# Kernel optimization log

Measured on AMD Instinct MI355X. Metric: run time of the kernel, lower is better.

The kernel has to match this reference:

```python
import jax, jax.numpy as jnp
import numpy as np

P, L, H = 3, 4, 6          # window size, num scales, num heads
EPS = 1e-5                 # LayerNorm eps (PyTorch default)


def setup_inputs() -> dict:
    key = jax.random.key(0)
    B, T, D = 8, 4096, 768
    ks = jax.random.split(key, 12)
    s = 0.02
    w = lambda k, shape: (jax.random.normal(k, shape, jnp.float32) * s)
    z = lambda n: jnp.zeros((n,), jnp.float32)
    return {
        "x": jax.random.normal(ks[0], (B, T, D), jnp.float32),
        "ln_g": jnp.ones((D,), jnp.float32),
        "ln_b": z(D),
        "qw": w(ks[1], (D, D)), "qb": z(D),
        "kw": w(ks[2], (D, D)), "kb": z(D),
        "vw": w(ks[3], (D, D)), "vb": z(D),
        "inw": w(ks[4], (3 * D, D)), "inb": z(3 * D),   # MHA in_proj
        "mow": w(ks[5], (D, D)), "mob": z(D),            # MHA out_proj
        "ow": w(ks[6], (D, D)), "ob": z(D),              # output_proj
    }


def _layernorm(x, g, b):
    mu = jnp.mean(x, -1, keepdims=True)
    var = jnp.mean((x - mu) ** 2, -1, keepdims=True)
    return (x - mu) * jax.lax.rsqrt(var + EPS) * g + b


def _mha_windows(q, k, v, inw, inb, mow, mob):
    # q,k,v: [B, W, P, D] -- batched tiny attention over all windows at once
    B, W, Pw, D = q.shape
    hd = D // H
    wq, wk, wv = inw[:D], inw[D:2 * D], inw[2 * D:]
    bq, bk, bv = inb[:D], inb[D:2 * D], inb[2 * D:]
    qp = (q @ wq.T + bq).reshape(B, W, Pw, H, hd)
    kp = (k @ wk.T + bk).reshape(B, W, Pw, H, hd)
    vp = (v @ wv.T + bv).reshape(B, W, Pw, H, hd)
    scores = jnp.einsum('bwqhd,bwkhd->bwhqk', qp, kp) / jnp.sqrt(jnp.float32(hd))
    attn = jax.nn.softmax(scores, axis=-1)
    o = jnp.einsum('bwhqk,bwkhd->bwqhd', attn, vp).reshape(B, W, Pw, D)
    return o @ mow.T + mob


def reference(x, ln_g, ln_b, qw, qb, kw, kb, vw, vb, inw, inb, mow, mob, ow, ob):
    B, T, D = x.shape
    xn = _layernorm(x, ln_g, ln_b)
    Q = xn @ qw.T + qb
    K = xn @ kw.T + kb
    V = xn @ vw.T + vb
    acc = jnp.zeros_like(x)
    for kk in range(L):
        scale = P ** kk
        if T < scale:
            continue
        Lp = T // scale
        pool = lambda z: z[:, :Lp * scale].reshape(B, Lp, scale, D).mean(axis=2)
        pQ, pK, pV = pool(Q), pool(K), pool(V)
        W = Lp // P
        if W == 0:
            continue
        win = lambda z: z[:, :W * P].reshape(B, W, P, D)
        o = _mha_windows(win(pQ), win(pK), win(pV), inw, inb, mow, mob)
        so = o.reshape(B, W * P, D)                       # concat of windows
        idx = (jnp.arange(T) * (W * P)) // T              # nearest interp to T
        up = so[:, idx]
        acc = acc + jax.nn.gelu(up, approximate=False)    # exact GELU (torch default)
    out = acc @ ow.T + ob
    return x + out
```

## Files before the change

kernel.cpp:

```cpp
#include <hip/hip_runtime.h>
#include <stdint.h>

typedef short s16x8 __attribute__((ext_vector_type(8)));
typedef float f32x4 __attribute__((ext_vector_type(4)));

__device__ __forceinline__ unsigned short f2bf(float f) {
  unsigned u = __builtin_bit_cast(unsigned, f);
  u = (u + 0x7FFFu + ((u >> 16) & 1u)) >> 16;
  return (unsigned short)u;
}
__device__ __forceinline__ float bf2f(unsigned short h) {
  unsigned u = ((unsigned)h) << 16;
  return __builtin_bit_cast(float, u);
}

__device__ __forceinline__ void gload_lds16(const void* g, void* l) {
  __builtin_amdgcn_global_load_lds((__attribute__((address_space(1))) void*)g,
                                   (__attribute__((address_space(3))) void*)l,
                                   16, 0, 0);
}

__global__ __launch_bounds__(256)
void mstr_prep(const float* __restrict__ qw, const float* __restrict__ kw,
               const float* __restrict__ vw, const float* __restrict__ inw,
               const float* __restrict__ mow, const float* __restrict__ ow,
               const float* __restrict__ inb, const float* __restrict__ qb,
               const float* __restrict__ kb, const float* __restrict__ vb,
               unsigned short* __restrict__ inwB, unsigned short* __restrict__ wT,
               unsigned short* __restrict__ mowB, unsigned short* __restrict__ owB,
               float* __restrict__ bc, float* __restrict__ zb)
{
  const long n1 = 589824;
  __shared__ float tile[32][33];
  int b = blockIdx.x, tid = threadIdx.x;
  if (b < 11520) {
    long i = (long)b * 256 + tid;
    if (i < 3 * n1)      inwB[i] = f2bf(inw[i]);
    else if (i < 4 * n1) mowB[i - 3 * n1] = f2bf(mow[i - 3 * n1]);
    else                 owB[i - 4 * n1] = f2bf(ow[i - 4 * n1]);
  } else if (b < 13248) {
    int z = b - 11520;
    int s = z % 3, r = z / 3;
    int jb = r % 24, kb = r / 24;
    const float* src = (s == 0) ? qw : (s == 1) ? kw : vw;
    unsigned short* dst = wT + (long)s * n1;
    int tx = tid & 31, ty = tid >> 5;
    int j0 = jb * 32, k0 = kb * 32;
#pragma unroll
    for (int i = 0; i < 4; ++i)
      tile[ty + i * 8][tx] = src[(long)(j0 + ty + i * 8) * 768 + k0 + tx];
    __syncthreads();
#pragma unroll
    for (int i = 0; i < 4; ++i)
      dst[(long)(k0 + ty + i * 8) * 768 + j0 + tx] = f2bf(tile[tx][ty + i * 8]);
  } else {
    int gid = (b - 13248) * 256 + tid;
    if (gid < 768) zb[gid] = 0.f;
    int s = gid / 768, c = gid - s * 768;
    const float* bb = (s == 0) ? qb : (s == 1) ? kb : vb;
    const float* wrow = inw + (long)(s * 768 + c) * 768;
    float a = inb[s * 768 + c];
    for (int j = 0; j < 768; ++j) a += bb[j] * wrow[j];
    bc[gid] = a;
  }
}

__global__ __launch_bounds__(256)
void mstr_ln(const float* __restrict__ x, const float* __restrict__ g,
             const float* __restrict__ bt, unsigned short* __restrict__ xn)
{
  int blk = blockIdx.x;
  int bb = blk / 4095, t = blk - bb * 4095;
  const float* xr = x + ((long)bb * 4096 + t) * 768;
  unsigned short* orow = xn + (long)blk * 768;
  int tid = threadIdx.x;
  float v0 = xr[tid], v1 = xr[tid + 256], v2 = xr[tid + 512];
  float s = v0 + v1 + v2;
  float s2 = v0 * v0 + v1 * v1 + v2 * v2;
#pragma unroll
  for (int o = 32; o > 0; o >>= 1) { s += __shfl_down(s, o, 64); s2 += __shfl_down(s2, o, 64); }
  __shared__ float rs[4], rq[4];
  int lane = tid & 63, wid = tid >> 6;
  if (lane == 0) { rs[wid] = s; rq[wid] = s2; }
  __syncthreads();
  float S = rs[0] + rs[1] + rs[2] + rs[3];
  float S2 = rq[0] + rq[1] + rq[2] + rq[3];
  float mu = S * (1.0f / 768.0f);
  float var = S2 * (1.0f / 768.0f) - mu * mu;
  float rstd = rsqrtf(var + 1e-5f);
  __builtin_nontemporal_store(f2bf((v0 - mu) * rstd * g[tid] + bt[tid]), &orow[tid]);
  __builtin_nontemporal_store(f2bf((v1 - mu) * rstd * g[tid + 256] + bt[tid + 256]), &orow[tid + 256]);
  __builtin_nontemporal_store(f2bf((v2 - mu) * rstd * g[tid + 512] + bt[tid + 512]), &orow[tid + 512]);
}

template<int EPI>
__global__ __launch_bounds__(256, 4)
void mstr_gemm(const unsigned short* __restrict__ A, int M,
               const unsigned short* __restrict__ W,
               const float* __restrict__ bias,
               unsigned short* out0, unsigned short* out1, unsigned short* out2,
               float* outf, const float* xadd,
               int rowDiv, int rowStride, int NC, int nwg, long zoff)
{
  __shared__ char smem[49152];
  if (zoff) {
    long zo = (long)blockIdx.y * zoff;
    A += zo; W += zo; out0 += zo; out1 += zo; out2 += zo;
  }
  int orig = blockIdx.x;
  int swq = nwg >> 3, swr = nwg & 7;
  int xcd = orig & 7, sidx = orig >> 3;
  int wg = (xcd < swr ? xcd * (swq + 1) : swr * (swq + 1) + (xcd - swr) * swq) + sidx;
  int rowp = wg / NC, colp = wg - rowp * NC;

  const int tid = threadIdx.x;
  const int lane = tid & 63;
  const int wid = tid >> 6;
  const int wr = wid >> 1, wc = wid & 1;
  const long row0 = (long)rowp * 128;
  const int col0 = colp * 128;

  const int sr = tid >> 2;
  const int sc = (((tid & 3) ^ ((tid >> 3) & 3)) << 3);
  long a0r = row0 + sr;       if (a0r >= M) a0r = M - 1;
  long a1r = row0 + sr + 64;  if (a1r >= M) a1r = M - 1;
  const unsigned short* Ag0 = A + a0r * 768 + sc;
  const unsigned short* Ag1 = A + a1r * 768 + sc;
  const unsigned short* Bg0 = W + (long)(col0 + sr) * 768 + sc;
  const unsigned short* Bg1 = W + (long)(col0 + sr + 64) * 768 + sc;
  char* ldsT = smem + tid * 16;

  const int fr = lane & 15;
  const int g4 = lane >> 4;
  const int cx = ((g4 ^ ((fr >> 1) & 3)) << 4);
  const int aoff = (wr * 64 + fr) * 64 + cx;
  const int boff = 8192 + (wc * 64 + fr) * 64 + cx;

  f32x4 acc[4][4] = {};

#define MSTAGE(T, BO) { \
    gload_lds16(Ag0 + (T) * 32, ldsT + (BO)); \
    gload_lds16(Ag1 + (T) * 32, ldsT + (BO) + 4096); \
    gload_lds16(Bg0 + (T) * 32, ldsT + (BO) + 8192); \
    gload_lds16(Bg1 + (T) * 32, ldsT + (BO) + 12288); }

#define STEP(T) { \
    if ((T) < 23) { \
      MSTAGE((T) + 1, (((T) + 1) % 3) * 16384) \
      asm volatile("s_waitcnt vmcnt(4)" ::: "memory"); \
    } else { \
      asm volatile("s_waitcnt vmcnt(0)" ::: "memory"); \
    } \
    __builtin_amdgcn_s_barrier(); \
    { \
      const char* sb_ = smem + ((T) % 3) * 16384; \
      s16x8 af[4], bfv[4]; \
      _Pragma("unroll") \
      for (int m = 0; m < 4; ++m) af[m] = *(const s16x8*)(sb_ + aoff + m * 1024); \
      _Pragma("unroll") \
      for (int n = 0; n < 4; ++n) bfv[n] = *(const s16x8*)(sb_ + boff + n * 1024); \
      __builtin_amdgcn_s_setprio(1); \
      _Pragma("unroll") \
      for (int m = 0; m < 4; ++m) \
        _Pragma("unroll") \
        for (int n = 0; n < 4; ++n) \
          acc[m][n] = __builtin_amdgcn_mfma_f32_16x16x32_bf16(af[m], bfv[n], acc[m][n], 0, 0, 0); \
      __builtin_amdgcn_s_setprio(0); \
    } }

  MSTAGE(0, 0)
  STEP(0)  STEP(1)  STEP(2)  STEP(3)  STEP(4)  STEP(5)
  STEP(6)  STEP(7)  STEP(8)  STEP(9)  STEP(10) STEP(11)
  STEP(12) STEP(13) STEP(14) STEP(15) STEP(16) STEP(17)
  STEP(18) STEP(19) STEP(20) STEP(21) STEP(22) STEP(23)
#undef STEP
#undef MSTAGE

  int seg = (col0 >= 1536) ? 2 : (col0 >= 768 ? 1 : 0);
  unsigned short* outp = (seg == 0) ? out0 : (seg == 1) ? out1 : out2;
  int csub = seg * 768;
#pragma unroll
  for (int m = 0; m < 4; ++m) {
#pragma unroll
    for (int r = 0; r < 4; ++r) {
      long gr = row0 + wr * 64 + m * 16 + g4 * 4 + r;
      if (gr < M) {
        long orow;
        if (EPI == 1) {
          orow = gr;
        } else {
          int qq = (int)gr / rowDiv;
          orow = (long)qq * rowStride + ((int)gr - qq * rowDiv);
        }
#pragma unroll
        for (int n = 0; n < 4; ++n) {
          int c = col0 + wc * 64 + n * 16 + fr;
          float v = acc[m][n][r] + bias[c];
          if (EPI == 1) {
            long o = gr * 768 + c;
            __builtin_nontemporal_store(v + __builtin_nontemporal_load(&xadd[o]), &outf[o]);
          } else if (EPI == 2) {
            v = 0.5f * v * (1.0f + erff(v * 0.70710678118654752f));
            __builtin_nontemporal_store(f2bf(v), &outp[orow * 768 + (c - csub)]);
          } else {
            __builtin_nontemporal_store(f2bf(v), &outp[orow * 768 + (c - csub)]);
          }
        }
      }
    }
  }
}

__global__ __launch_bounds__(384)
void mstr_pool(unsigned short* qp, unsigned short* kp, unsigned short* vp,
               int srcOff, int dstOff, int Ndst)
{
  unsigned short* p = (blockIdx.y == 0) ? qp : (blockIdx.y == 1) ? kp : vp;
  int tok = blockIdx.x;
  int bb = tok / Ndst, j = tok - bb * Ndst;
  long sb = ((long)bb * 6063 + srcOff + 3 * j) * 768 + threadIdx.x * 2;
  long db = ((long)bb * 6063 + dstOff + j) * 768 + threadIdx.x * 2;
  unsigned a = *(const unsigned*)(p + sb);
  unsigned b = *(const unsigned*)(p + sb + 768);
  unsigned c = *(const unsigned*)(p + sb + 1536);
  float lo = (bf2f((unsigned short)a) + bf2f((unsigned short)b) + bf2f((unsigned short)c)) * (1.0f / 3.0f);
  float hi = (bf2f((unsigned short)(a >> 16)) + bf2f((unsigned short)(b >> 16)) + bf2f((unsigned short)(c >> 16))) * (1.0f / 3.0f);
  unsigned o = (unsigned)f2bf(lo) | ((unsigned)f2bf(hi) << 16);
  *(unsigned*)(p + db) = o;
}

__global__ __launch_bounds__(256)
void mstr_attn(unsigned short* qp, unsigned short* kp, unsigned short* vp, int nwaves)
{
  int gw = blockIdx.x * 4 + (threadIdx.x >> 6);
  if (gw >= nwaves) return;
  int lane = threadIdx.x & 63;
  int win = gw / 6, h = gw - win * 6;
  int bb = win / 2021, ww = win - bb * 2021;
  int row0;
  if (ww < 1365)      row0 = 3 * ww;
  else if (ww < 1820) row0 = 4095 + 3 * (ww - 1365);
  else if (ww < 1971) row0 = 5460 + 3 * (ww - 1820);
  else                row0 = 5913 + 3 * (ww - 1971);
  long base = ((long)bb * 6063 + row0) * 768 + h * 128 + lane * 2;
  float q[3][2], k[3][2], v[3][2];
#pragma unroll
  for (int i = 0; i < 3; ++i) {
    unsigned uq = *(const unsigned*)(qp + base + i * 768);
    unsigned uk = *(const unsigned*)(kp + base + i * 768);
    unsigned uv = *(const unsigned*)(vp + base + i * 768);
    q[i][0] = bf2f((unsigned short)uq); q[i][1] = bf2f((unsigned short)(uq >> 16));
    k[i][0] = bf2f((unsigned short)uk); k[i][1] = bf2f((unsigned short)(uk >> 16));
    v[i][0] = bf2f((unsigned short)uv); v[i][1] = bf2f((unsigned short)(uv >> 16));
  }
  float s[3][3];
#pragma unroll
  for (int i = 0; i < 3; ++i)
#pragma unroll
    for (int j = 0; j < 3; ++j)
      s[i][j] = q[i][0] * k[j][0] + q[i][1] * k[j][1];
#pragma unroll
  for (int st = 1; st < 64; st <<= 1) {
#pragma unroll
    for (int i = 0; i < 3; ++i)
#pragma unroll
      for (int j = 0; j < 3; ++j)
        s[i][j] += __shfl_xor(s[i][j], st, 64);
  }
  const float scl = 0.088388347648318447f;
#pragma unroll
  for (int i = 0; i < 3; ++i) {
    float s0 = s[i][0] * scl, s1 = s[i][1] * scl, s2 = s[i][2] * scl;
    float m = fmaxf(s0, fmaxf(s1, s2));
    float e0 = __expf(s0 - m), e1 = __expf(s1 - m), e2 = __expf(s2 - m);
    float inv = 1.0f / (e0 + e1 + e2);
    e0 *= inv; e1 *= inv; e2 *= inv;
    float o0 = e0 * v[0][0] + e1 * v[1][0] + e2 * v[2][0];
    float o1 = e0 * v[0][1] + e1 * v[1][1] + e2 * v[2][1];
    unsigned o = (unsigned)f2bf(o0) | ((unsigned)f2bf(o1) << 16);
    *(unsigned*)(qp + base + i * 768) = o;
  }
}

__global__ __launch_bounds__(256)
void mstr_gelusum(const unsigned short* __restrict__ omo, unsigned short* __restrict__ acc)
{
  long gid = (long)blockIdx.x * 256 + threadIdx.x;
  int d2 = (int)(gid % 384);
  long row = gid / 384;
  int bb = (int)(row >> 12);
  int t = (int)(row & 4095);
  const int NkA[4] = {4095, 1365, 453, 150};
  const int soA[4] = {0, 4095, 5460, 5913};
  float a0 = 0.f, a1 = 0.f;
#pragma unroll
  for (int kk = 0; kk < 4; ++kk) {
    int idx = (t * NkA[kk]) >> 12;
    long tok = (long)bb * 6063 + soA[kk] + idx;
    unsigned u = *(const unsigned*)(omo + tok * 768 + d2 * 2);
    a0 += bf2f((unsigned short)u);
    a1 += bf2f((unsigned short)(u >> 16));
  }
  unsigned o = (unsigned)f2bf(a0) | ((unsigned)f2bf(a1) << 16);
  *(unsigned*)(acc + row * 768 + d2 * 2) = o;
}

extern "C" void kernel_launch(void* const* d_in, const int* in_sizes, int n_in,
                              void* d_out, int out_size, void* d_ws, size_t ws_size,
                              hipStream_t stream)
{
  const float* x   = (const float*)d_in[0];
  const float* lng = (const float*)d_in[1];
  const float* lnb = (const float*)d_in[2];
  const float* qw  = (const float*)d_in[3];
  const float* qb  = (const float*)d_in[4];
  const float* kw  = (const float*)d_in[5];
  const float* kb  = (const float*)d_in[6];
  const float* vw  = (const float*)d_in[7];
  const float* vb  = (const float*)d_in[8];
  const float* inw = (const float*)d_in[9];
  const float* inb = (const float*)d_in[10];
  const float* mob = (const float*)d_in[12];
  const float* ow  = (const float*)d_in[13];
  const float* ob  = (const float*)d_in[14];

  const long n1 = 589824;
  char* ws = (char*)d_ws;
  size_t off = 0;
  auto alloc = [&](size_t bytes) -> char* {
    char* p = ws + off;
    off += (bytes + 255) & ~(size_t)255;
    return p;
  };
  unsigned short* Wc = (unsigned short*)alloc((size_t)5 * n1 * 2);
  float* bc = (float*)alloc(2304 * 4);
  float* zb = (float*)alloc(768 * 4);
  size_t fixed = off;

  int g = 0;
  const int cands[4] = {8, 4, 2, 1};
  for (int ci = 0; ci < 4; ++ci) {
    int c = cands[ci];
    size_t need = fixed + (size_t)c * 4096 * 768 * 2
                + 2 * (size_t)c * 6063 * 768 * 2
                + 1024;
    if (need <= ws_size) { g = c; break; }
  }
  if (!g) return;

  char* GR = ws + fixed;
  unsigned short* xnacc = (unsigned short*)GR;
  unsigned short* qp = xnacc + (size_t)g * 4096 * 768;
  unsigned short* kp = qp + (size_t)g * 6063 * 768;
  unsigned short* inwB = (unsigned short*)GR;
  unsigned short* wT   = inwB + 3 * n1;

  unsigned short* mowB = Wc + 3 * n1;
  unsigned short* owB  = Wc + 4 * n1;

  mstr_prep<<<dim3(13257), dim3(256), 0, stream>>>(qw, kw, vw, inw, (const float*)d_in[11], ow,
                                                   inb, qb, kb, vb, inwB, wT, mowB, owB, bc, zb);
  mstr_gemm<0><<<dim3(36, 3), dim3(256), 0, stream>>>(inwB, 768, wT, zb, Wc, Wc, Wc,
                                                      nullptr, nullptr, 768, 768, 6, 36, n1);

  int ng = 8 / g;
  for (int gi = 0; gi < ng; ++gi) {
    const float* xg = x + (long)gi * g * 4096 * 768;
    unsigned short* vp = (unsigned short*)d_out + (long)gi * g * 4096 * 768 * 2;
    mstr_ln<<<dim3(g * 4095), dim3(256), 0, stream>>>(xg, lng, lnb, xnacc);
    int M1 = g * 4095, gb1 = (M1 + 127) / 128;
    int nwg1 = gb1 * 18;
    mstr_gemm<0><<<dim3(nwg1), dim3(256), 0, stream>>>(xnacc, M1, Wc, bc,
                                                       qp, kp, vp, nullptr, nullptr,
                                                       4095, 6063, 18, nwg1, 0);
    mstr_pool<<<dim3(g * 1365, 3), dim3(384), 0, stream>>>(qp, kp, vp, 0, 4095, 1365);
    mstr_pool<<<dim3(g * 453, 3), dim3(384), 0, stream>>>(qp, kp, vp, 4095, 5460, 453);
    mstr_pool<<<dim3(g * 150, 3), dim3(384), 0, stream>>>(qp, kp, vp, 5460, 5913, 150);
    int nw = g * 2021 * 6;
    mstr_attn<<<dim3((nw + 3) / 4), dim3(256), 0, stream>>>(qp, kp, vp, nw);
    int M2 = g * 6063;
    int nwg2 = ((M2 + 127) / 128) * 6;
    mstr_gemm<2><<<dim3(nwg2), dim3(256), 0, stream>>>(qp, M2, mowB, mob, kp, kp, kp,
                                                       nullptr, nullptr, M2, 0, 6, nwg2, 0);
    mstr_gelusum<<<dim3(g * 6144), dim3(256), 0, stream>>>(kp, xnacc);
    int M3 = g * 4096;
    int nwg3 = (M3 / 128) * 6;
    mstr_gemm<1><<<dim3(nwg3), dim3(256), 0, stream>>>(xnacc, M3, owB, ob, nullptr, nullptr, nullptr,
                                                       (float*)d_out + (long)gi * g * 4096 * 768, xg,
                                                       M3, 0, 6, nwg3, 0);
  }
}
```

Measured before the change: 642.8 us.

## Fuse first LayerNorm into prep, merge pool launches, widen gelusum

Folds the first group's LayerNorm into the weight-prep kernel and moves the bf16 weight scratch into the qp buffer, so xnacc is not overwritten. Replaces three sequential pooling launches with one launch that pools directly from the level-0 rows with factors 3/9/27. gelusum now handles four bf16 values per thread with 8-byte loads and nontemporal stores. The intent is to cut launch count and serialization and to raise memory-access width. The cost is that the coarse pools now read more rows (9 and 27 instead of 3), and the result is rounded from different bf16 intermediates.

Measured after the change: 696.2 us. 1.08x slower.

```diff
diff --git a/kernel.cpp b/kernel.cpp
--- a/kernel.cpp
+++ b/kernel.cpp
@@ -3,6 +3,7 @@
 
 typedef short s16x8 __attribute__((ext_vector_type(8)));
 typedef float f32x4 __attribute__((ext_vector_type(4)));
+typedef unsigned u32x2 __attribute__((ext_vector_type(2)));
 
 __device__ __forceinline__ unsigned short f2bf(float f) {
   unsigned u = __builtin_bit_cast(unsigned, f);
@@ -12,6 +13,12 @@
 __device__ __forceinline__ float bf2f(unsigned short h) {
   unsigned u = ((unsigned)h) << 16;
   return __builtin_bit_cast(float, u);
+}
+__device__ __forceinline__ float bflo(unsigned u) {
+  return __builtin_bit_cast(float, u << 16);
+}
+__device__ __forceinline__ float bfhi(unsigned u) {
+  return __builtin_bit_cast(float, u & 0xFFFF0000u);
 }
 
 __device__ __forceinline__ void gload_lds16(const void* g, void* l) {
@@ -28,10 +35,13 @@
                const float* __restrict__ kb, const float* __restrict__ vb,
                unsigned short* __restrict__ inwB, unsigned short* __restrict__ wT,
                unsigned short* __restrict__ mowB, unsigned short* __restrict__ owB,
-               float* __restrict__ bc, float* __restrict__ zb)
+               float* __restrict__ bc, float* __restrict__ zb,
+               const float* __restrict__ x, const float* __restrict__ lng,
+               const float* __restrict__ lnb, unsigned short* __restrict__ xn)
 {
   const long n1 = 589824;
   __shared__ float tile[32][33];
+  __shared__ float rs[4], rq[4];
   int b = blockIdx.x, tid = threadIdx.x;
   if (b < 11520) {
     long i = (long)b * 256 + tid;
@@ -53,7 +63,7 @@
 #pragma unroll
     for (int i = 0; i < 4; ++i)
       dst[(long)(k0 + ty + i * 8) * 768 + j0 + tx] = f2bf(tile[tx][ty + i * 8]);
-  } else {
+  } else if (b < 13257) {
     int gid = (b - 13248) * 256 + tid;
     if (gid < 768) zb[gid] = 0.f;
     int s = gid / 768, c = gid - s * 768;
@@ -62,6 +72,27 @@
     float a = inb[s * 768 + c];
     for (int j = 0; j < 768; ++j) a += bb[j] * wrow[j];
     bc[gid] = a;
+  } else {
+    int blk = b - 13257;
+    int bb = blk / 4095, t = blk - bb * 4095;
+    const float* xr = x + ((long)bb * 4096 + t) * 768;
+    unsigned short* orow = xn + (long)blk * 768;
+    float v0 = xr[tid], v1 = xr[tid + 256], v2 = xr[tid + 512];
+    float s = v0 + v1 + v2;
+    float s2 = v0 * v0 + v1 * v1 + v2 * v2;
+#pragma unroll
+    for (int o = 32; o > 0; o >>= 1) { s += __shfl_down(s, o, 64); s2 += __shfl_down(s2, o, 64); }
+    int lane = tid & 63, wid = tid >> 6;
+    if (lane == 0) { rs[wid] = s; rq[wid] = s2; }
+    __syncthreads();
+    float S = rs[0] + rs[1] + rs[2] + rs[3];
+    float S2 = rq[0] + rq[1] + rq[2] + rq[3];
+    float mu = S * (1.0f / 768.0f);
+    float var = S2 * (1.0f / 768.0f) - mu * mu;
+    float rstd = rsqrtf(var + 1e-5f);
+    __builtin_nontemporal_store(f2bf((v0 - mu) * rstd * lng[tid] + lnb[tid]), &orow[tid]);
+    __builtin_nontemporal_store(f2bf((v1 - mu) * rstd * lng[tid + 256] + lnb[tid + 256]), &orow[tid + 256]);
+    __builtin_nontemporal_store(f2bf((v2 - mu) * rstd * lng[tid + 512] + lnb[tid + 512]), &orow[tid + 512]);
   }
 }
 
@@ -212,21 +243,25 @@
 }
 
 __global__ __launch_bounds__(384)
-void mstr_pool(unsigned short* qp, unsigned short* kp, unsigned short* vp,
-               int srcOff, int dstOff, int Ndst)
+void mstr_pool(unsigned short* qp, unsigned short* kp, unsigned short* vp)
 {
   unsigned short* p = (blockIdx.y == 0) ? qp : (blockIdx.y == 1) ? kp : vp;
   int tok = blockIdx.x;
-  int bb = tok / Ndst, j = tok - bb * Ndst;
-  long sb = ((long)bb * 6063 + srcOff + 3 * j) * 768 + threadIdx.x * 2;
-  long db = ((long)bb * 6063 + dstOff + j) * 768 + threadIdx.x * 2;
-  unsigned a = *(const unsigned*)(p + sb);
-  unsigned b = *(const unsigned*)(p + sb + 768);
-  unsigned c = *(const unsigned*)(p + sb + 1536);
-  float lo = (bf2f((unsigned short)a) + bf2f((unsigned short)b) + bf2f((unsigned short)c)) * (1.0f / 3.0f);
-  float hi = (bf2f((unsigned short)(a >> 16)) + bf2f((unsigned short)(b >> 16)) + bf2f((unsigned short)(c >> 16))) * (1.0f / 3.0f);
-  unsigned o = (unsigned)f2bf(lo) | ((unsigned)f2bf(hi) << 16);
-  *(unsigned*)(p + db) = o;
+  int bb = tok / 1968, r = tok - bb * 1968;
+  int j, F, dstOff;
+  if (r < 1365)      { j = r;        F = 3;  dstOff = 4095; }
+  else if (r < 1818) { j = r - 1365; F = 9;  dstOff = 5460; }
+  else               { j = r - 1818; F = 27; dstOff = 5913; }
+  long srcB = ((long)bb * 6063 + (long)j * F) * 768 + threadIdx.x * 2;
+  long dstB = ((long)bb * 6063 + dstOff + j) * 768 + threadIdx.x * 2;
+  float lo = 0.f, hi = 0.f;
+  for (int i = 0; i < F; ++i) {
+    unsigned u = *(const unsigned*)(p + srcB + (long)i * 768);
+    lo += bflo(u); hi += bfhi(u);
+  }
+  float inv = 1.0f / (float)F;
+  unsigned o = (unsigned)f2bf(lo * inv) | ((unsigned)f2bf(hi * inv) << 16);
+  *(unsigned*)(p + dstB) = o;
 }
 
 __global__ __launch_bounds__(256)
@@ -249,9 +284,9 @@
     unsigned uq = *(const unsigned*)(qp + base + i * 768);
     unsigned uk = *(const unsigned*)(kp + base + i * 768);
     unsigned uv = *(const unsigned*)(vp + base + i * 768);
-    q[i][0] = bf2f((unsigned short)uq); q[i][1] = bf2f((unsigned short)(uq >> 16));
-    k[i][0] = bf2f((unsigned short)uk); k[i][1] = bf2f((unsigned short)(uk >> 16));
-    v[i][0] = bf2f((unsigned short)uv); v[i][1] = bf2f((unsigned short)(uv >> 16));
+    q[i][0] = bflo(uq); q[i][1] = bfhi(uq);
+    k[i][0] = bflo(uk); k[i][1] = bfhi(uk);
+    v[i][0] = bflo(uv); v[i][1] = bfhi(uv);
   }
   float s[3][3];
 #pragma unroll
@@ -286,23 +321,25 @@
 void mstr_gelusum(const unsigned short* __restrict__ omo, unsigned short* __restrict__ acc)
 {
   long gid = (long)blockIdx.x * 256 + threadIdx.x;
-  int d2 = (int)(gid % 384);
-  long row = gid / 384;
+  int d4 = (int)(gid % 192);
+  long row = gid / 192;
   int bb = (int)(row >> 12);
   int t = (int)(row & 4095);
   const int NkA[4] = {4095, 1365, 453, 150};
   const int soA[4] = {0, 4095, 5460, 5913};
-  float a0 = 0.f, a1 = 0.f;
+  float a0 = 0.f, a1 = 0.f, a2 = 0.f, a3 = 0.f;
 #pragma unroll
   for (int kk = 0; kk < 4; ++kk) {
     int idx = (t * NkA[kk]) >> 12;
     long tok = (long)bb * 6063 + soA[kk] + idx;
-    unsigned u = *(const unsigned*)(omo + tok * 768 + d2 * 2);
-    a0 += bf2f((unsigned short)u);
-    a1 += bf2f((unsigned short)(u >> 16));
-  }
-  unsigned o = (unsigned)f2bf(a0) | ((unsigned)f2bf(a1) << 16);
-  *(unsigned*)(acc + row * 768 + d2 * 2) = o;
+    u32x2 u = *(const u32x2*)(omo + tok * 768 + d4 * 4);
+    a0 += bflo(u.x); a1 += bfhi(u.x);
+    a2 += bflo(u.y); a3 += bfhi(u.y);
+  }
+  u32x2 o;
+  o.x = (unsigned)f2bf(a0) | ((unsigned)f2bf(a1) << 16);
+  o.y = (unsigned)f2bf(a2) | ((unsigned)f2bf(a3) << 16);
+  __builtin_nontemporal_store(o, (u32x2*)(acc + row * 768 + d4 * 4));
 }
 
 extern "C" void kernel_launch(void* const* d_in, const int* in_sizes, int n_in,
@@ -352,14 +389,17 @@
   unsigned short* xnacc = (unsigned short*)GR;
   unsigned short* qp = xnacc + (size_t)g * 4096 * 768;
   unsigned short* kp = qp + (size_t)g * 6063 * 768;
-  unsigned short* inwB = (unsigned short*)GR;
-  unsigned short* wT   = inwB + 3 * n1;
+  unsigned short* inwB = qp;
+  unsigned short* wT   = qp + 3 * n1;
 
   unsigned short* mowB = Wc + 3 * n1;
   unsigned short* owB  = Wc + 4 * n1;
 
-  mstr_prep<<<dim3(13257), dim3(256), 0, stream>>>(qw, kw, vw, inw, (const float*)d_in[11], ow,
-                                                   inb, qb, kb, vb, inwB, wT, mowB, owB, bc, zb);
+  int nLN0 = g * 4095;
+  mstr_prep<<<dim3(13257 + nLN0), dim3(256), 0, stream>>>(
+      qw, kw, vw, inw, (const float*)d_in[11], ow,
+      inb, qb, kb, vb, inwB, wT, mowB, owB, bc, zb,
+      x, lng, lnb, xnacc);
   mstr_gemm<0><<<dim3(36, 3), dim3(256), 0, stream>>>(inwB, 768, wT, zb, Wc, Wc, Wc,
                                                       nullptr, nullptr, 768, 768, 6, 36, n1);
 
@@ -367,22 +407,21 @@
   for (int gi = 0; gi < ng; ++gi) {
     const float* xg = x + (long)gi * g * 4096 * 768;
     unsigned short* vp = (unsigned short*)d_out + (long)gi * g * 4096 * 768 * 2;
-    mstr_ln<<<dim3(g * 4095), dim3(256), 0, stream>>>(xg, lng, lnb, xnacc);
+    if (gi > 0)
+      mstr_ln<<<dim3(g * 4095), dim3(256), 0, stream>>>(xg, lng, lnb, xnacc);
     int M1 = g * 4095, gb1 = (M1 + 127) / 128;
     int nwg1 = gb1 * 18;
     mstr_gemm<0><<<dim3(nwg1), dim3(256), 0, stream>>>(xnacc, M1, Wc, bc,
                                                        qp, kp, vp, nullptr, nullptr,
                                                        4095, 6063, 18, nwg1, 0);
-    mstr_pool<<<dim3(g * 1365, 3), dim3(384), 0, stream>>>(qp, kp, vp, 0, 4095, 1365);
-    mstr_pool<<<dim3(g * 453, 3), dim3(384), 0, stream>>>(qp, kp, vp, 4095, 5460, 453);
-    mstr_pool<<<dim3(g * 150, 3), dim3(384), 0, stream>>>(qp, kp, vp, 5460, 5913, 150);
+    mstr_pool<<<dim3(g * 1968, 3), dim3(384), 0, stream>>>(qp, kp, vp);
     int nw = g * 2021 * 6;
     mstr_attn<<<dim3((nw + 3) / 4), dim3(256), 0, stream>>>(qp, kp, vp, nw);
     int M2 = g * 6063;
     int nwg2 = ((M2 + 127) / 128) * 6;
     mstr_gemm<2><<<dim3(nwg2), dim3(256), 0, stream>>>(qp, M2, mowB, mob, kp, kp, kp,
                                                        nullptr, nullptr, M2, 0, 6, nwg2, 0);
-    mstr_gelusum<<<dim3(g * 6144), dim3(256), 0, stream>>>(kp, xnacc);
+    mstr_gelusum<<<dim3(g * 3072), dim3(256), 0, stream>>>(kp, xnacc);
     int M3 = g * 4096;
     int nwg3 = (M3 / 128) * 6;
     mstr_gemm<1><<<dim3(nwg3), dim3(256), 0, stream>>>(xnacc, M3, owB, ob, nullptr, nullptr, nullptr,
```
